# Kernel optimization log

Hardware: AMD Instinct MI355X
Metric: run time of the kernel (lower is better)

## Reference

```python
import jax, jax.numpy as jnp
import numpy as np

DIM = 64       # feature_dim
EDIM = 4       # edge_dim
EH = 128       # edge MLP hidden
MDIM = 64      # message dim


def _glorot(key, shape):
    fan_in = shape[0]
    return jax.random.normal(key, shape, dtype=jnp.float32) / jnp.sqrt(jnp.float32(fan_in))


def setup_inputs() -> dict:
    key = jax.random.key(0)
    ks = jax.random.split(key, 16)
    B, N = 8, 384
    feats = jax.random.normal(ks[0], (B, N, DIM), dtype=jnp.float32)
    coors = jax.random.normal(ks[1], (B, N, 3), dtype=jnp.float32)
    vel = jax.random.normal(ks[2], (B, N, 3), dtype=jnp.float32)
    edges = jax.random.normal(ks[3], (B, N, N, EDIM), dtype=jnp.float32)
    e_in = 2 * DIM + 1 + EDIM  # [h_i, h_j, ||x_i-x_j||^2, e_ij]
    params = dict(
        We1=_glorot(ks[4], (e_in, EH)), be1=jnp.zeros((EH,), jnp.float32),
        We2=_glorot(ks[5], (EH, MDIM)), be2=jnp.zeros((MDIM,), jnp.float32),
        Wc1=_glorot(ks[6], (MDIM, MDIM)), bc1=jnp.zeros((MDIM,), jnp.float32),
        Wc2=_glorot(ks[7], (MDIM, 1)), bc2=jnp.zeros((1,), jnp.float32),
        Wn1=_glorot(ks[8], (DIM + MDIM, 2 * DIM)), bn1=jnp.zeros((2 * DIM,), jnp.float32),
        Wn2=_glorot(ks[9], (2 * DIM, DIM)), bn2=jnp.zeros((DIM,), jnp.float32),
        Wv=_glorot(ks[10], (DIM, 1)), bv=jnp.zeros((1,), jnp.float32),
    )
    return dict(feats=feats, coors=coors, vel=vel, edges=edges, **params)


def _egnn(feats, coors, vel, edges, We1, be1, We2, be2, Wc1, bc1, Wc2, bc2,
          Wn1, bn1, Wn2, bn2, Wv, bv):
    B, N, _ = feats.shape
    # pairwise relative coordinates and squared distances
    rel = coors[:, :, None, :] - coors[:, None, :, :]            # [B,N,N,3]
    dist2 = jnp.sum(rel * rel, axis=-1, keepdims=True)           # [B,N,N,1]
    hi = jnp.broadcast_to(feats[:, :, None, :], (B, N, N, DIM))
    hj = jnp.broadcast_to(feats[:, None, :, :], (B, N, N, DIM))
    e_in = jnp.concatenate([hi, hj, dist2, edges], axis=-1)      # [B,N,N,2d+1+e]
    m = jax.nn.silu(e_in @ We1 + be1)
    m = jax.nn.silu(m @ We2 + be2)                                # [B,N,N,MDIM]
    # coordinate weights (scalar per edge)
    cw = jax.nn.silu(m @ Wc1 + bc1) @ Wc2 + bc2                   # [B,N,N,1]
    agg = jnp.mean(rel * cw, axis=2)                              # [B,N,3]
    # velocity update: vel' = phi_vel(h) * vel + agg ; coors' = coors + vel'
    gate = feats @ Wv + bv                                        # [B,N,1]
    vel_new = gate * vel + agg
    coors_new = coors + vel_new
    # node update with summed messages, residual
    m_i = jnp.sum(m, axis=2)                                      # [B,N,MDIM]
    h = jnp.concatenate([feats, m_i], axis=-1)
    h = jax.nn.silu(h @ Wn1 + bn1) @ Wn2 + bn2
    feats_new = feats + h
    return feats_new, coors_new, vel_new


def reference(feats, coors, vel, edges, We1, be1, We2, be2, Wc1, bc1, Wc2, bc2,
              Wn1, bn1, Wn2, bn2, Wv, bv):
    t, c, v = _egnn(feats, coors, vel, edges, We1, be1, We2, be2, Wc1, bc1,
                    Wc2, bc2, Wn1, bn1, Wn2, bn2, Wv, bv)
    return (t, jax.nn.selu(c), jax.nn.selu(v))
```

## Files before the change

### kernel.cpp

```cpp
#include <hip/hip_runtime.h>
#include <hip/hip_bf16.h>
#include <cstdint>

#define NN 384
#define OUT1OFF 196608
#define OUT2OFF 205824

typedef float f4 __attribute__((ext_vector_type(4)));
typedef short short8 __attribute__((ext_vector_type(8)));
typedef unsigned int u32;

union FragU { short8 s; u32 w[4]; };

__device__ inline unsigned short f2bf(float f) {
    u32 u = __float_as_uint(f);
    return (unsigned short)((u + 0x7fffu + ((u >> 16) & 1u)) >> 16);
}
__device__ inline u32 pkbf(float lo, float hi) {
    u32 r;
    asm("v_cvt_pk_bf16_f32 %0, %1, %2" : "=v"(r) : "v"(lo), "v"(hi));
    return r;
}
__device__ inline float siluf(float x) {
    return x * __builtin_amdgcn_rcpf(1.0f + __expf(-x));
}
__device__ inline float seluf(float x) {
    const float sc = 1.0507009873554805f, al = 1.6732632423543772f;
    return x > 0.f ? sc * x : sc * al * (__expf(x) - 1.f);
}

#define DSFENCE() do { asm volatile("s_waitcnt lgkmcnt(0)" ::: "memory"); \
                       __builtin_amdgcn_sched_barrier(0); } while (0)

__global__ __launch_bounds__(128) void egnn_prep1(
    const float* __restrict__ feats, const float* __restrict__ We1,
    const float* __restrict__ be1, float* __restrict__ HiC, float* __restrict__ HjC) {
    int r0 = blockIdx.x * 8;
    int t = threadIdx.x;
    __shared__ float fr[8][64];
    for (int k = t; k < 512; k += 128) fr[k >> 6][k & 63] = feats[(size_t)r0 * 64 + k];
    __syncthreads();
    float a1[8], a2[8];
#pragma unroll
    for (int r = 0; r < 8; r++) { a1[r] = be1[t]; a2[r] = 0.f; }
    for (int d = 0; d < 64; d++) {
        float w1 = We1[d * 128 + t], w2 = We1[(64 + d) * 128 + t];
#pragma unroll
        for (int r = 0; r < 8; r++) { a1[r] += fr[r][d] * w1; a2[r] += fr[r][d] * w2; }
    }
#pragma unroll
    for (int r = 0; r < 8; r++) {
        HiC[(size_t)(r0 + r) * 128 + t] = a1[r];
        HjC[(size_t)(r0 + r) * 128 + t] = a2[r];
    }
}

__global__ __launch_bounds__(64) void egnn_prep2(
    const float* __restrict__ We2, const float* __restrict__ Wc1,
    unsigned short* __restrict__ B2P, unsigned short* __restrict__ B3P) {
    int f = blockIdx.x;
    int l = threadIdx.x;
    int g = l >> 4, cc = l & 15;
    if (f < 16) {
        int n = f >> 2, ks = f & 3;
#pragma unroll
        for (int e = 0; e < 8; e++) {
            int row = ks * 32 + 8 * g + e, col = n * 16 + cc;
            B2P[(f * 64 + l) * 8 + e] = f2bf(We2[row * 64 + col]);
        }
    } else {
        int f2 = f - 16;
        int n = f2 >> 1, k2 = f2 & 1;
#pragma unroll
        for (int e = 0; e < 8; e++) {
            int row = k2 * 32 + 8 * g + e, col = n * 16 + cc;
            B3P[(f2 * 64 + l) * 8 + e] = f2bf(Wc1[row * 64 + col]);
        }
    }
}

__global__ __launch_bounds__(256, 2) void egnn_main(
    const float* __restrict__ feats, const float* __restrict__ coors,
    const float* __restrict__ vel, const float* __restrict__ edges,
    const float* __restrict__ We1,
    const float* __restrict__ be2, const float* __restrict__ bc1,
    const float* __restrict__ Wc2, const float* __restrict__ bc2,
    const float* __restrict__ Wn1, const float* __restrict__ bn1,
    const float* __restrict__ Wn2, const float* __restrict__ bn2,
    const float* __restrict__ Wv, const float* __restrict__ bv,
    const float* __restrict__ HiC, const float* __restrict__ HjC,
    const unsigned short* __restrict__ B2P, const unsigned short* __restrict__ B3P,
    float* __restrict__ out) {
    __shared__ __align__(16) short xch[4][16][136];

    const int tid = threadIdx.x;
    const int w = tid >> 6, lane = tid & 63;
    const int g = lane >> 4, c = lane & 15;

    const int blk = blockIdx.x;
    const int sw = (blk & 7) * 96 + (blk >> 3);
    const int flat = sw * 4 + w;
    const int b = flat / NN;
    const size_t bi = (size_t)flat;

    short8 b2f[4][4], b3f[4][2];
#pragma unroll
    for (int n = 0; n < 4; n++)
#pragma unroll
        for (int ks = 0; ks < 4; ks++)
            b2f[n][ks] = *(const short8*)(B2P + ((n * 4 + ks) * 64 + lane) * 8);
#pragma unroll
    for (int n = 0; n < 4; n++)
#pragma unroll
        for (int k2 = 0; k2 < 2; k2++)
            b3f[n][k2] = *(const short8*)(B3P + ((n * 2 + k2) * 64 + lane) * 8);

    u32 w1p0[8], w1p1[8], w1p2[8];
#pragma unroll
    for (int n = 0; n < 8; n++) {
        float v0 = 0.f, v1 = 0.f, v2 = 0.f, v3 = 0.f, v4 = 0.f, v5 = 0.f;
        if (g == 0) {
            const int h = n * 16 + c;
            v0 = We1[128 * 128 + h]; v1 = We1[129 * 128 + h];
            v2 = We1[130 * 128 + h]; v3 = We1[131 * 128 + h];
            v4 = We1[132 * 128 + h];
            v5 = HiC[bi * 128 + h];
        }
        w1p0[n] = pkbf(v0, v1);
        w1p1[n] = pkbf(v2, v3);
        w1p2[n] = pkbf(v4, v5);
    }

    const float bc2v = bc2[0];
    const float ci0 = coors[bi * 3], ci1 = coors[bi * 3 + 1], ci2 = coors[bi * 3 + 2];
    const float cig = (g == 0) ? ci0 : ((g == 1) ? ci1 : ci2);

    f4 maccv[4];
#pragma unroll
    for (int n = 0; n < 4; n++) maccv[n] = (f4){0.f, 0.f, 0.f, 0.f};
    float aggp = 0.f;

    short* xrow = &xch[w][c][0];

#pragma unroll 1
    for (int jt = 0; jt < 24; ++jt) {
        const int j = jt * 16 + c;
        const float* cjp = &coors[((size_t)b * NN + j) * 3];
        const float cj0 = cjp[0], cj1 = cjp[1], cj2 = cjp[2];
        const f4 ev = *(const f4*)&edges[(bi * NN + j) * 4];
        const float* hjp = &HjC[((size_t)b * NN + j) * 128];
        const float r0 = ci0 - cj0, r1 = ci1 - cj1, r2 = ci2 - cj2;
        const float d2v = r0 * r0 + r1 * r1 + r2 * r2;

        FragU b1;
        b1.w[0] = (g == 0) ? pkbf(d2v, ev.x) : 0u;
        b1.w[1] = (g == 0) ? pkbf(ev.y, ev.z) : 0u;
        b1.w[2] = (g == 0) ? pkbf(ev.w, 1.0f) : 0u;
        b1.w[3] = 0u;

#pragma unroll
        for (int n = 0; n < 8; n++) {
            FragU a1;
            a1.w[0] = w1p0[n]; a1.w[1] = w1p1[n]; a1.w[2] = w1p2[n]; a1.w[3] = 0u;
            const f4 hcn = *(const f4*)&hjp[n * 16 + 4 * g];
            f4 d1 = __builtin_amdgcn_mfma_f32_16x16x32_bf16(a1.s, b1.s, hcn, 0, 0, 0);
            const u32 lo = pkbf(siluf(d1.x), siluf(d1.y));
            const u32 hi = pkbf(siluf(d1.z), siluf(d1.w));
            *(uint2*)&xrow[n * 16 + 4 * g] = make_uint2(lo, hi);
        }
        DSFENCE();

        f4 c2[4];
#pragma unroll
        for (int n = 0; n < 4; n++) c2[n] = *(const f4*)&be2[n * 16 + 4 * g];
#pragma unroll
        for (int ks = 0; ks < 4; ks++) {
            const short8 b2 = *(const short8*)&xrow[ks * 32 + 8 * g];
#pragma unroll
            for (int n = 0; n < 4; n++)
                c2[n] = __builtin_amdgcn_mfma_f32_16x16x32_bf16(b2f[n][ks], b2, c2[n], 0, 0, 0);
        }
#pragma unroll
        for (int n = 0; n < 4; n++) {
            f4 s2;
            s2.x = siluf(c2[n].x); s2.y = siluf(c2[n].y);
            s2.z = siluf(c2[n].z); s2.w = siluf(c2[n].w);
            maccv[n] += s2;
            *(uint2*)&xrow[n * 16 + 4 * g] = make_uint2(pkbf(s2.x, s2.y), pkbf(s2.z, s2.w));
        }
        DSFENCE();

        f4 c3[4];
#pragma unroll
        for (int n = 0; n < 4; n++) c3[n] = *(const f4*)&bc1[n * 16 + 4 * g];
#pragma unroll
        for (int k2 = 0; k2 < 2; k2++) {
            const short8 b3 = *(const short8*)&xrow[k2 * 32 + 8 * g];
#pragma unroll
            for (int n = 0; n < 4; n++)
                c3[n] = __builtin_amdgcn_mfma_f32_16x16x32_bf16(b3f[n][k2], b3, c3[n], 0, 0, 0);
        }
        float cwp = 0.f;
#pragma unroll
        for (int n = 0; n < 4; n++) {
            const f4 wc = *(const f4*)&Wc2[n * 16 + 4 * g];
            cwp += siluf(c3[n].x) * wc.x;
            cwp += siluf(c3[n].y) * wc.y;
            cwp += siluf(c3[n].z) * wc.z;
            cwp += siluf(c3[n].w) * wc.w;
        }
        cwp += __shfl_xor(cwp, 16);
        cwp += __shfl_xor(cwp, 32);
        const float cw = cwp + bc2v;
        const float cjg = (g == 0) ? cj0 : ((g == 1) ? cj1 : cj2);
        aggp += (cig - cjg) * cw;
    }

    DSFENCE();
    float* red = (float*)&xch[w][0][0];
    float* hid = red + 128;

#pragma unroll
    for (int n = 0; n < 4; n++) {
#pragma unroll
        for (int r = 0; r < 4; r++) {
            float v = maccv[n][r];
            v += __shfl_xor(v, 1); v += __shfl_xor(v, 2);
            v += __shfl_xor(v, 4); v += __shfl_xor(v, 8);
            maccv[n][r] = v;
        }
    }
    const float fv = feats[bi * 64 + lane];
    float gp = fv * Wv[lane];
    gp += __shfl_xor(gp, 1);  gp += __shfl_xor(gp, 2);
    gp += __shfl_xor(gp, 4);  gp += __shfl_xor(gp, 8);
    gp += __shfl_xor(gp, 16); gp += __shfl_xor(gp, 32);
    const float sgate = gp + bv[0];

    float aggr = aggp;
    aggr += __shfl_xor(aggr, 1); aggr += __shfl_xor(aggr, 2);
    aggr += __shfl_xor(aggr, 4); aggr += __shfl_xor(aggr, 8);

    red[lane] = fv;
    if (c == 0) {
#pragma unroll
        for (int n = 0; n < 4; n++)
            *(f4*)&red[64 + n * 16 + 4 * g] = maccv[n];
    }
    DSFENCE();

    float a0 = bn1[lane], a1 = bn1[64 + lane];
#pragma unroll 4
    for (int k0 = 0; k0 < 128; k0 += 4) {
        const f4 rv = *(const f4*)&red[k0];
#pragma unroll
        for (int kk = 0; kk < 4; kk++) {
            const float* wr = &Wn1[(size_t)(k0 + kk) * 128];
            a0 += rv[kk] * wr[lane];
            a1 += rv[kk] * wr[64 + lane];
        }
    }
    hid[lane] = siluf(a0);
    hid[64 + lane] = siluf(a1);
    DSFENCE();
    float o = bn2[lane];
#pragma unroll 4
    for (int k0 = 0; k0 < 128; k0 += 4) {
        const f4 hv = *(const f4*)&hid[k0];
#pragma unroll
        for (int kk = 0; kk < 4; kk++)
            o += hv[kk] * Wn2[(size_t)(k0 + kk) * 64 + lane];
    }
    out[bi * 64 + lane] = fv + o;

    if (c == 0 && g < 3) {
        const size_t base = bi * 3 + g;
        const float vn = sgate * vel[base] + aggr * (1.f / 384.f);
        const float cn = coors[base] + vn;
        out[OUT1OFF + base] = seluf(cn);
        out[OUT2OFF + base] = seluf(vn);
    }
}

extern "C" void kernel_launch(void* const* d_in, const int* in_sizes, int n_in,
                              void* d_out, int out_size, void* d_ws, size_t ws_size,
                              hipStream_t stream) {
    const float* feats = (const float*)d_in[0];
    const float* coors = (const float*)d_in[1];
    const float* vel   = (const float*)d_in[2];
    const float* edges = (const float*)d_in[3];
    const float* We1   = (const float*)d_in[4];
    const float* be1   = (const float*)d_in[5];
    const float* We2   = (const float*)d_in[6];
    const float* be2   = (const float*)d_in[7];
    const float* Wc1   = (const float*)d_in[8];
    const float* bc1   = (const float*)d_in[9];
    const float* Wc2   = (const float*)d_in[10];
    const float* bc2   = (const float*)d_in[11];
    const float* Wn1   = (const float*)d_in[12];
    const float* bn1   = (const float*)d_in[13];
    const float* Wn2   = (const float*)d_in[14];
    const float* bn2   = (const float*)d_in[15];
    const float* Wv    = (const float*)d_in[16];
    const float* bv    = (const float*)d_in[17];

    float* HiC = (float*)d_ws;
    float* HjC = HiC + 393216;
    unsigned short* B2P = (unsigned short*)(HjC + 393216);
    unsigned short* B3P = B2P + 8192;
    float* out = (float*)d_out;

    egnn_prep1<<<384, 128, 0, stream>>>(feats, We1, be1, HiC, HjC);
    egnn_prep2<<<24, 64, 0, stream>>>(We2, Wc1, B2P, B3P);
    egnn_main<<<768, 256, 0, stream>>>(feats, coors, vel, edges, We1,
                                       be2, bc1, Wc2, bc2, Wn1, bn1, Wn2, bn2,
                                       Wv, bv, HiC, HjC, B2P, B3P, out);
}
```

Measured before the change: 144.4 us.

## Keep MLP activations in registers by permuting weight fragments, drop LDS exchange

The prep kernel now permutes the K ordering of the We2 and Wc1 bf16 fragments so that the MFMA output layout of one layer lines up with the B-operand layout of the next. Activations can then be repacked in registers instead of going through shared memory and fences between layers. The main kernel also moves to one wave per block (3072 blocks of 64 threads) with a new block-to-row mapping, and it prefetches the next tile's edge and coordinate values. The trade-off is higher register pressure and different occupancy and scheduling behaviour from the smaller blocks.

```diff
diff --git a/kernel.cpp b/kernel.cpp
--- a/kernel.cpp
+++ b/kernel.cpp
@@ -62,24 +62,24 @@
     int l = threadIdx.x;
     int g = l >> 4, cc = l & 15;
     if (f < 16) {
-        int n = f >> 2, ks = f & 3;
+        int nn = f >> 2, kk = f & 3;
 #pragma unroll
         for (int e = 0; e < 8; e++) {
-            int row = ks * 32 + 8 * g + e, col = n * 16 + cc;
-            B2P[(f * 64 + l) * 8 + e] = f2bf(We2[row * 64 + col]);
+            int h = (2 * kk + (e >> 2)) * 16 + 4 * g + (e & 3);
+            B2P[(f * 64 + l) * 8 + e] = f2bf(We2[h * 64 + nn * 16 + cc]);
         }
     } else {
         int f2 = f - 16;
-        int n = f2 >> 1, k2 = f2 & 1;
+        int mm = f2 >> 1, kk2 = f2 & 1;
 #pragma unroll
         for (int e = 0; e < 8; e++) {
-            int row = k2 * 32 + 8 * g + e, col = n * 16 + cc;
-            B3P[(f2 * 64 + l) * 8 + e] = f2bf(Wc1[row * 64 + col]);
-        }
-    }
-}
-
-__global__ __launch_bounds__(256, 2) void egnn_main(
+            int hm = (2 * kk2 + (e >> 2)) * 16 + 4 * g + (e & 3);
+            B3P[(f2 * 64 + l) * 8 + e] = f2bf(Wc1[hm * 64 + mm * 16 + cc]);
+        }
+    }
+}
+
+__global__ __launch_bounds__(64) void egnn_main(
     const float* __restrict__ feats, const float* __restrict__ coors,
     const float* __restrict__ vel, const float* __restrict__ edges,
     const float* __restrict__ We1,
@@ -91,29 +91,27 @@
     const float* __restrict__ HiC, const float* __restrict__ HjC,
     const unsigned short* __restrict__ B2P, const unsigned short* __restrict__ B3P,
     float* __restrict__ out) {
-    __shared__ __align__(16) short xch[4][16][136];
-
-    const int tid = threadIdx.x;
-    const int w = tid >> 6, lane = tid & 63;
+    __shared__ __align__(16) float epi[256];
+
+    const int lane = threadIdx.x;
     const int g = lane >> 4, c = lane & 15;
 
     const int blk = blockIdx.x;
-    const int sw = (blk & 7) * 96 + (blk >> 3);
-    const int flat = sw * 4 + w;
-    const int b = flat / NN;
+    const int flat = (blk & 7) * 384 + (blk >> 3);
+    const int b = blk & 7;
     const size_t bi = (size_t)flat;
 
-    short8 b2f[4][4], b3f[4][2];
-#pragma unroll
-    for (int n = 0; n < 4; n++)
-#pragma unroll
-        for (int ks = 0; ks < 4; ks++)
-            b2f[n][ks] = *(const short8*)(B2P + ((n * 4 + ks) * 64 + lane) * 8);
-#pragma unroll
-    for (int n = 0; n < 4; n++)
-#pragma unroll
-        for (int k2 = 0; k2 < 2; k2++)
-            b3f[n][k2] = *(const short8*)(B3P + ((n * 2 + k2) * 64 + lane) * 8);
+    FragU b2f[4][4], b3f[4][2];
+#pragma unroll
+    for (int nn = 0; nn < 4; nn++)
+#pragma unroll
+        for (int kk = 0; kk < 4; kk++)
+            b2f[nn][kk].s = *(const short8*)(B2P + ((nn * 4 + kk) * 64 + lane) * 8);
+#pragma unroll
+    for (int mm = 0; mm < 4; mm++)
+#pragma unroll
+        for (int kk2 = 0; kk2 < 2; kk2++)
+            b3f[mm][kk2].s = *(const short8*)(B3P + ((mm * 2 + kk2) * 64 + lane) * 8);
 
     u32 w1p0[8], w1p1[8], w1p2[8];
 #pragma unroll
@@ -140,74 +138,80 @@
     for (int n = 0; n < 4; n++) maccv[n] = (f4){0.f, 0.f, 0.f, 0.f};
     float aggp = 0.f;
 
-    short* xrow = &xch[w][c][0];
+    f4 ev = *(const f4*)&edges[(bi * NN + c) * 4];
+    const float* cjp0 = &coors[((size_t)b * NN + c) * 3];
+    float cjn0 = cjp0[0], cjn1 = cjp0[1], cjn2 = cjp0[2];
 
 #pragma unroll 1
     for (int jt = 0; jt < 24; ++jt) {
+        const f4 evc = ev;
+        const float cj0 = cjn0, cj1 = cjn1, cj2 = cjn2;
+        const int jn = (jt + 1 < 24) ? (jt + 1) * 16 + c : c;
+        ev = *(const f4*)&edges[(bi * NN + jn) * 4];
+        const float* cjp = &coors[((size_t)b * NN + jn) * 3];
+        cjn0 = cjp[0]; cjn1 = cjp[1]; cjn2 = cjp[2];
+
         const int j = jt * 16 + c;
-        const float* cjp = &coors[((size_t)b * NN + j) * 3];
-        const float cj0 = cjp[0], cj1 = cjp[1], cj2 = cjp[2];
-        const f4 ev = *(const f4*)&edges[(bi * NN + j) * 4];
         const float* hjp = &HjC[((size_t)b * NN + j) * 128];
         const float r0 = ci0 - cj0, r1 = ci1 - cj1, r2 = ci2 - cj2;
         const float d2v = r0 * r0 + r1 * r1 + r2 * r2;
 
         FragU b1;
-        b1.w[0] = (g == 0) ? pkbf(d2v, ev.x) : 0u;
-        b1.w[1] = (g == 0) ? pkbf(ev.y, ev.z) : 0u;
-        b1.w[2] = (g == 0) ? pkbf(ev.w, 1.0f) : 0u;
+        b1.w[0] = (g == 0) ? pkbf(d2v, evc.x) : 0u;
+        b1.w[1] = (g == 0) ? pkbf(evc.y, evc.z) : 0u;
+        b1.w[2] = (g == 0) ? pkbf(evc.w, 1.0f) : 0u;
         b1.w[3] = 0u;
 
+        FragU bf[4];
 #pragma unroll
         for (int n = 0; n < 8; n++) {
             FragU a1;
             a1.w[0] = w1p0[n]; a1.w[1] = w1p1[n]; a1.w[2] = w1p2[n]; a1.w[3] = 0u;
             const f4 hcn = *(const f4*)&hjp[n * 16 + 4 * g];
             f4 d1 = __builtin_amdgcn_mfma_f32_16x16x32_bf16(a1.s, b1.s, hcn, 0, 0, 0);
-            const u32 lo = pkbf(siluf(d1.x), siluf(d1.y));
-            const u32 hi = pkbf(siluf(d1.z), siluf(d1.w));
-            *(uint2*)&xrow[n * 16 + 4 * g] = make_uint2(lo, hi);
-        }
-        DSFENCE();
+            const int kk = n >> 1, ws = (n & 1) * 2;
+            bf[kk].w[ws]     = pkbf(siluf(d1.x), siluf(d1.y));
+            bf[kk].w[ws + 1] = pkbf(siluf(d1.z), siluf(d1.w));
+        }
 
         f4 c2[4];
 #pragma unroll
-        for (int n = 0; n < 4; n++) c2[n] = *(const f4*)&be2[n * 16 + 4 * g];
-#pragma unroll
-        for (int ks = 0; ks < 4; ks++) {
-            const short8 b2 = *(const short8*)&xrow[ks * 32 + 8 * g];
-#pragma unroll
-            for (int n = 0; n < 4; n++)
-                c2[n] = __builtin_amdgcn_mfma_f32_16x16x32_bf16(b2f[n][ks], b2, c2[n], 0, 0, 0);
-        }
-#pragma unroll
-        for (int n = 0; n < 4; n++) {
+        for (int nn = 0; nn < 4; nn++) c2[nn] = *(const f4*)&be2[nn * 16 + 4 * g];
+#pragma unroll
+        for (int kk = 0; kk < 4; kk++)
+#pragma unroll
+            for (int nn = 0; nn < 4; nn++)
+                c2[nn] = __builtin_amdgcn_mfma_f32_16x16x32_bf16(b2f[nn][kk].s, bf[kk].s, c2[nn], 0, 0, 0);
+
+        FragU bt[2];
+#pragma unroll
+        for (int nn = 0; nn < 4; nn++) {
             f4 s2;
-            s2.x = siluf(c2[n].x); s2.y = siluf(c2[n].y);
-            s2.z = siluf(c2[n].z); s2.w = siluf(c2[n].w);
-            maccv[n] += s2;
-            *(uint2*)&xrow[n * 16 + 4 * g] = make_uint2(pkbf(s2.x, s2.y), pkbf(s2.z, s2.w));
-        }
-        DSFENCE();
+            s2.x = siluf(c2[nn].x); s2.y = siluf(c2[nn].y);
+            s2.z = siluf(c2[nn].z); s2.w = siluf(c2[nn].w);
+            maccv[nn] += s2;
+            const int kk2 = nn >> 1, ws = (nn & 1) * 2;
+            bt[kk2].w[ws]     = pkbf(s2.x, s2.y);
+            bt[kk2].w[ws + 1] = pkbf(s2.z, s2.w);
+        }
 
         f4 c3[4];
 #pragma unroll
-        for (int n = 0; n < 4; n++) c3[n] = *(const f4*)&bc1[n * 16 + 4 * g];
-#pragma unroll
-        for (int k2 = 0; k2 < 2; k2++) {
-            const short8 b3 = *(const short8*)&xrow[k2 * 32 + 8 * g];
-#pragma unroll
-            for (int n = 0; n < 4; n++)
-                c3[n] = __builtin_amdgcn_mfma_f32_16x16x32_bf16(b3f[n][k2], b3, c3[n], 0, 0, 0);
-        }
+        for (int mm = 0; mm < 4; mm++) c3[mm] = *(const f4*)&bc1[mm * 16 + 4 * g];
+#pragma unroll
+        for (int kk2 = 0; kk2 < 2; kk2++)
+#pragma unroll
+            for (int mm = 0; mm < 4; mm++)
+                c3[mm] = __builtin_amdgcn_mfma_f32_16x16x32_bf16(b3f[mm][kk2].s, bt[kk2].s, c3[mm], 0, 0, 0);
+
         float cwp = 0.f;
 #pragma unroll
-        for (int n = 0; n < 4; n++) {
-            const f4 wc = *(const f4*)&Wc2[n * 16 + 4 * g];
-            cwp += siluf(c3[n].x) * wc.x;
-            cwp += siluf(c3[n].y) * wc.y;
-            cwp += siluf(c3[n].z) * wc.z;
-            cwp += siluf(c3[n].w) * wc.w;
+        for (int mm = 0; mm < 4; mm++) {
+            const f4 wc = *(const f4*)&Wc2[mm * 16 + 4 * g];
+            cwp += siluf(c3[mm].x) * wc.x;
+            cwp += siluf(c3[mm].y) * wc.y;
+            cwp += siluf(c3[mm].z) * wc.z;
+            cwp += siluf(c3[mm].w) * wc.w;
         }
         cwp += __shfl_xor(cwp, 16);
         cwp += __shfl_xor(cwp, 32);
@@ -216,9 +220,8 @@
         aggp += (cig - cjg) * cw;
     }
 
-    DSFENCE();
-    float* red = (float*)&xch[w][0][0];
-    float* hid = red + 128;
+    float* red = epi;
+    float* hid = epi + 128;
 
 #pragma unroll
     for (int n = 0; n < 4; n++) {
@@ -312,7 +315,7 @@
 
     egnn_prep1<<<384, 128, 0, stream>>>(feats, We1, be1, HiC, HjC);
     egnn_prep2<<<24, 64, 0, stream>>>(We2, Wc1, B2P, B3P);
-    egnn_main<<<768, 256, 0, stream>>>(feats, coors, vel, edges, We1,
+    egnn_main<<<3072, 64, 0, stream>>>(feats, coors, vel, edges, We1,
                                        be2, bc1, Wc2, bc2, Wn1, bn1, Wn2, bn2,
                                        Wv, bv, HiC, HjC, B2P, B3P, out);
 }
```

Result: slower. 170.8 us (+18.2%).
